# Kernel tuning notes

Hardware: AMD Instinct MI355X
Metric: run time of the kernel (lower is better)

The kernel has to match this reference:

```python
import jax, jax.numpy as jnp
import numpy as np

N = 50000   # total nodes in batched graph
E = 400000  # directed edges
G = 512     # number of graphs in batch
F = 128     # input node feature dim
K = 4       # attention heads
H = 64      # hidden feats per head (flatten width = K*H = 256)
EPS = 1e-5  # BatchNorm eps


def _edge_softmax(e, dst, n):
    # softmax of per-edge scores over incoming edges of each dst node; e: [E, K]
    m = jax.ops.segment_max(e, dst, num_segments=n)
    ee = jnp.exp(e - m[dst])
    s = jax.ops.segment_sum(ee, dst, num_segments=n)
    return ee / s[dst]


def _gat_layer(x, W, al, ar, b, resW, src, dst, agg):
    # dgl GATConv with residual=True, LeakyReLU(0.2), bias, ReLU activation
    n = x.shape[0]
    z = (x @ W).reshape(n, K, H)                      # [N, K, H]
    el = jnp.einsum('nkh,kh->nk', z, al)              # [N, K]
    er = jnp.einsum('nkh,kh->nk', z, ar)
    e = jax.nn.leaky_relu(el[src] + er[dst], negative_slope=0.2)  # [E, K]
    a = _edge_softmax(e, dst, n)                      # [E, K]
    rst = jax.ops.segment_sum(a[:, :, None] * z[src], dst, num_segments=n)  # [N, K, H]
    res = (x @ resW).reshape(n, K, H) if resW is not None else x.reshape(n, K, H)
    rst = jax.nn.relu(rst + res + b.reshape(1, K, H))
    return rst.reshape(n, K * H) if agg == 'flatten' else rst.mean(axis=1)


def setup_inputs() -> dict:
    key = jax.random.key(0)
    ks = jax.random.split(key, 16)
    f32 = jnp.float32

    def p(k, shape):
        return jax.random.normal(k, shape, f32) * 0.1

    h = jax.random.normal(ks[0], (N, F), f32)
    src = jax.random.randint(ks[1], (E,), 0, N)
    dst = jax.random.randint(ks[2], (E,), 0, N)
    graph_ids = (jnp.arange(N) * G) // N  # sorted node->graph assignment, all segments nonempty

    return dict(
        h=h, src=src, dst=dst, graph_ids=graph_ids,
        W0=p(ks[3], (F, K * H)), al0=p(ks[4], (K, H)), ar0=p(ks[5], (K, H)),
        b0=jnp.zeros((K * H,), f32), resW0=p(ks[6], (F, K * H)),
        W1=p(ks[7], (K * H, K * H)), al1=p(ks[8], (K, H)), ar1=p(ks[9], (K, H)),
        b1=jnp.zeros((K * H,), f32),
        W2=p(ks[10], (K * H, K * H)), al2=p(ks[11], (K, H)), ar2=p(ks[12], (K, H)),
        b2=jnp.zeros((K * H,), f32),
        Wg=p(ks[13], (H, 1)), bg=jnp.zeros((1,), f32),
        Wm1=p(ks[14], (2 * H, H)), bm1=jnp.zeros((H,), f32),
        bn_g=jnp.ones((H,), f32), bn_b=jnp.zeros((H,), f32),
        bn_m=jnp.zeros((H,), f32), bn_v=jnp.ones((H,), f32),
        Wm2=p(ks[15], (H, 1)), bm2=jnp.zeros((1,), f32),
    )


def reference(h, src, dst, graph_ids, W0, al0, ar0, b0, resW0, W1, al1, ar1, b1,
              W2, al2, ar2, b2, Wg, bg, Wm1, bm1, bn_g, bn_b, bn_m, bn_v, Wm2, bm2):
    # 3 GAT layers: flatten, flatten, mean (dgllife GATPredictor default agg modes)
    x = _gat_layer(h, W0, al0, ar0, b0, resW0, src, dst, 'flatten')   # [N, 256]
    x = _gat_layer(x, W1, al1, ar1, b1, None, src, dst, 'flatten')    # [N, 256] (identity residual)
    x = _gat_layer(x, W2, al2, ar2, b2, None, src, dst, 'mean')       # [N, 64]
    # WeightedSumAndMax readout
    w = jax.nn.sigmoid(x @ Wg + bg)                                   # [N, 1]
    gs = jax.ops.segment_sum(w * x, graph_ids, num_segments=G)        # [G, 64]
    gm = jax.ops.segment_max(x, graph_ids, num_segments=G)            # [G, 64]
    gf = jnp.concatenate([gs, gm], axis=1)                            # [G, 128]
    # MLPPredictor (eval mode: dropout off, BatchNorm uses running stats)
    y = jax.nn.relu(gf @ Wm1 + bm1)
    y = (y - bn_m) / jnp.sqrt(bn_v + EPS) * bn_g + bn_b
    out = jax.nn.sigmoid(y @ Wm2 + bm2)                               # [G, 1]
    return out
```

## Files before the change

kernel.cpp:

```cpp
#include <hip/hip_runtime.h>
#include <math.h>


typedef _Float16 f16;
typedef _Float16 f16x4 __attribute__((ext_vector_type(4)));
typedef _Float16 f16x8 __attribute__((ext_vector_type(8)));
typedef float f32x16 __attribute__((ext_vector_type(16)));

__device__ __forceinline__ double wred_sumd(double v) {
#pragma unroll
  for (int m = 32; m > 0; m >>= 1) v += __shfl_xor(v, m, 64);
  return v;
}

__global__ void k_hist(const int* __restrict__ dst, int* __restrict__ deg, int e) {
  int i = blockIdx.x * 256 + threadIdx.x;
  if (i < e) atomicAdd(&deg[dst[i]], 1);
}

__global__ void k_scan1(const int* __restrict__ deg, int* __restrict__ rowptr,
                        int* __restrict__ bsum, int n) {
  __shared__ int sh[256];
  int t = threadIdx.x;
  int base = blockIdx.x * 1024 + t * 4;
  int v0 = 0, v1 = 0, v2 = 0, v3 = 0;
  if (base + 0 < n) v0 = deg[base + 0];
  if (base + 1 < n) v1 = deg[base + 1];
  if (base + 2 < n) v2 = deg[base + 2];
  if (base + 3 < n) v3 = deg[base + 3];
  sh[t] = v0 + v1 + v2 + v3;
  __syncthreads();
  for (int off = 1; off < 256; off <<= 1) {
    int x = (t >= off) ? sh[t - off] : 0;
    __syncthreads();
    sh[t] += x;
    __syncthreads();
  }
  int excl = (t > 0) ? sh[t - 1] : 0;
  if (base + 0 < n) rowptr[base + 0] = excl;
  if (base + 1 < n) rowptr[base + 1] = excl + v0;
  if (base + 2 < n) rowptr[base + 2] = excl + v0 + v1;
  if (base + 3 < n) rowptr[base + 3] = excl + v0 + v1 + v2;
  if (t == 255) bsum[blockIdx.x] = sh[255];
}

__global__ void k_scan2(int* bsum, int nb) {
  if (threadIdx.x == 0 && blockIdx.x == 0) {
    int run = 0;
    for (int i = 0; i < nb; i++) { int v = bsum[i]; bsum[i] = run; run += v; }
  }
}

__global__ void k_scan3(int* __restrict__ rowptr, const int* __restrict__ bsum,
                        int n, int e) {
  int i = blockIdx.x * 256 + threadIdx.x;
  if (i < n) rowptr[i] += bsum[i >> 10];
  if (i == 0) rowptr[n] = e;
}

__global__ void k_scatter(const int* __restrict__ src, const int* __restrict__ dst,
                          const int* __restrict__ rowptr, int* __restrict__ cursor,
                          int* __restrict__ colsrc, int e) {
  int i = blockIdx.x * 256 + threadIdx.x;
  if (i < e) {
    int d = dst[i];
    int pos = rowptr[d] + atomicAdd(&cursor[d], 1);
    colsrc[pos] = src[i];
  }
}

__global__ __launch_bounds__(256) void k_split(const float* __restrict__ X,
                                               f16* __restrict__ X0,
                                               f16* __restrict__ X1, int n4) {
  int i = blockIdx.x * 256 + threadIdx.x;
  if (i >= n4) return;
  float4 v = *(const float4*)(X + (size_t)i * 4);
  f16x4 hi, lo;
  hi.x = (f16)v.x; lo.x = (f16)(v.x - (float)hi.x);
  hi.y = (f16)v.y; lo.y = (f16)(v.y - (float)hi.y);
  hi.z = (f16)v.z; lo.z = (f16)(v.z - (float)hi.z);
  hi.w = (f16)v.w; lo.w = (f16)(v.w - (float)hi.w);
  *(f16x4*)(X0 + (size_t)i * 4) = hi;
  *(f16x4*)(X1 + (size_t)i * 4) = lo;
}

__global__ void k_splitWT(const float* __restrict__ W, f16* __restrict__ P0,
                          f16* __restrict__ P1, int kin) {
  int c = blockIdx.x;
  for (int k = threadIdx.x; k < kin; k += blockDim.x) {
    float v = W[(size_t)k * 256 + c];
    f16 h0 = (f16)v;
    size_t off = ((size_t)(k >> 4) * 256 + c) * 16 + ((k >> 3) & 1) * 8 + (k & 7);
    P0[off] = h0;
    P1[off] = (f16)(v - (float)h0);
  }
}

template <int KIN, bool ELR>
__global__ __launch_bounds__(256) void k_gemm_mfma(
    const f16* __restrict__ X0, const f16* __restrict__ X1,
    const f16* __restrict__ WT0, const f16* __restrict__ WT1,
    float* __restrict__ C, const float* __restrict__ al,
    const float* __restrict__ ar, float* __restrict__ el,
    float* __restrict__ er, int M) {
  __shared__ f16 aLDS[2][2][64][8];
  const int t = threadIdx.x;
  const int w = t >> 6;
  const int lane = t & 63;
  const int lo = lane & 31, g = lane >> 5;
  const int row0 = blockIdx.x * 32;

  f32x16 acc0, acc1;
#pragma unroll
  for (int i = 0; i < 16; i++) { acc0[i] = 0.f; acc1[i] = 0.f; }

  const size_t fb0 = (size_t)(w * 64 + lo) * 16 + g * 8;
  const size_t fb1 = (size_t)(w * 64 + 32 + lo) * 16 + g * 8;

  for (int k0 = 0; k0 < KIN; k0 += 32) {
    if (k0) __syncthreads();
    {
      int s = t >> 7, r = (t >> 2) & 31, hh = t & 3;
      int kh = hh >> 1, gg = hh & 1;
      int gr = row0 + r;
      if (gr > M - 1) gr = M - 1;
      const f16* Xs = s ? X1 : X0;
      *(float4*)&aLDS[s][kh][(gg << 5) | r][0] =
          *(const float4*)&Xs[(size_t)gr * KIN + k0 + kh * 16 + gg * 8];
    }
    __syncthreads();
#pragma unroll
    for (int kh = 0; kh < 2; kh++) {
      const size_t bbase = (size_t)((k0 >> 4) + kh) * 4096;
      f16x8 a0 = *(const f16x8*)&aLDS[0][kh][lane][0];
      f16x8 a1 = *(const f16x8*)&aLDS[1][kh][lane][0];
      f16x8 b0c0 = *(const f16x8*)&WT0[bbase + fb0];
      f16x8 b0c1 = *(const f16x8*)&WT0[bbase + fb1];
      f16x8 b1c0 = *(const f16x8*)&WT1[bbase + fb0];
      f16x8 b1c1 = *(const f16x8*)&WT1[bbase + fb1];
      acc0 = __builtin_amdgcn_mfma_f32_32x32x16_f16(a0, b0c0, acc0, 0, 0, 0);
      acc1 = __builtin_amdgcn_mfma_f32_32x32x16_f16(a0, b0c1, acc1, 0, 0, 0);
      acc0 = __builtin_amdgcn_mfma_f32_32x32x16_f16(a0, b1c0, acc0, 0, 0, 0);
      acc1 = __builtin_amdgcn_mfma_f32_32x32x16_f16(a0, b1c1, acc1, 0, 0, 0);
      acc0 = __builtin_amdgcn_mfma_f32_32x32x16_f16(a1, b0c0, acc0, 0, 0, 0);
      acc1 = __builtin_amdgcn_mfma_f32_32x32x16_f16(a1, b0c1, acc1, 0, 0, 0);
    }
  }
  const int c0 = w * 64 + lo, c1 = w * 64 + 32 + lo;
#pragma unroll
  for (int reg = 0; reg < 16; reg++) {
    int rr = (reg & 3) + 8 * (reg >> 2) + 4 * g;
    int r0 = row0 + rr;
    if (r0 < M) {
      C[(size_t)r0 * 256 + c0] = acc0[reg];
      C[(size_t)r0 * 256 + c1] = acc1[reg];
    }
  }
  if (ELR) {
    __syncthreads();
    int r = t & 31, kk = (t >> 5) & 3, sel = t >> 7;
    int gr = row0 + r;
    if (gr < M) {
      const float* zr = C + (size_t)gr * 256 + kk * 64;
      const float* av = (sel ? ar : al) + kk * 64;
      float s = 0.f;
#pragma unroll
      for (int q = 0; q < 16; q++) {
        float4 zv = *(const float4*)(zr + q * 4);
        float4 a4 = *(const float4*)(av + q * 4);
        s += zv.x * a4.x + zv.y * a4.y + zv.z * a4.z + zv.w * a4.w;
      }
      (sel ? er : el)[gr * 4 + kk] = s;
    }
  }
}

template <int MEAN, int RESF16>
__global__ __launch_bounds__(256) void k_gather(
    const float* __restrict__ z, const float* __restrict__ el,
    const float* __restrict__ er, const float* __restrict__ resf,
    const f16* __restrict__ R0, const f16* __restrict__ R1,
    const float* __restrict__ bias, const int* __restrict__ rowptr,
    const int* __restrict__ colsrc, float* __restrict__ out,
    f16* __restrict__ O0, f16* __restrict__ O1, float* __restrict__ wn,
    const float* __restrict__ Wg, const float* __restrict__ bg, int n) {
  const int t = threadIdx.x;
  const int w = t >> 6, lane = t & 63;
  int node = blockIdx.x * 4 + w;
  if (node > n - 1) node = n - 1;
  const int base = rowptr[node];
  const int deg = rowptr[node + 1] - base;
  const int k = lane >> 4, j = lane & 15;
  const float ernk = er[node * 4 + k];

  float m = -INFINITY;
  for (int i0 = 0; i0 < deg; i0 += 16) {
    int i = i0 + j;
    if (i < deg) {
      int s = colsrc[base + i];
      float sc = el[s * 4 + k] + ernk;
      sc = (sc > 0.f) ? sc : 0.2f * sc;
      m = fmaxf(m, sc);
    }
  }
#pragma unroll
  for (int msk = 1; msk < 16; msk <<= 1) m = fmaxf(m, __shfl_xor(m, msk, 64));

  float ssum = 0.f;
  for (int i0 = 0; i0 < deg; i0 += 16) {
    int i = i0 + j;
    if (i < deg) {
      int s = colsrc[base + i];
      float sc = el[s * 4 + k] + ernk;
      sc = (sc > 0.f) ? sc : 0.2f * sc;
      ssum += expf(sc - m);
    }
  }
#pragma unroll
  for (int msk = 1; msk < 16; msk <<= 1) ssum += __shfl_xor(ssum, msk, 64);
  const float inv = 1.f / ssum;

  const char* zb = (const char*)z + lane * 16;
  float4 acc0 = {0, 0, 0, 0}, acc1 = {0, 0, 0, 0};
  float4 acc2 = {0, 0, 0, 0}, acc3 = {0, 0, 0, 0};
  int i = 0;
  for (; i + 4 <= deg; i += 4) {
    int s0 = colsrc[base + i + 0];
    int s1 = colsrc[base + i + 1];
    int s2 = colsrc[base + i + 2];
    int s3 = colsrc[base + i + 3];
    float4 z0 = *(const float4*)(zb + ((size_t)s0 << 10));
    float4 z1 = *(const float4*)(zb + ((size_t)s1 << 10));
    float4 z2 = *(const float4*)(zb + ((size_t)s2 << 10));
    float4 z3 = *(const float4*)(zb + ((size_t)s3 << 10));
    float c0 = el[s0 * 4 + k] + ernk; c0 = (c0 > 0.f) ? c0 : 0.2f * c0;
    float c1 = el[s1 * 4 + k] + ernk; c1 = (c1 > 0.f) ? c1 : 0.2f * c1;
    float c2 = el[s2 * 4 + k] + ernk; c2 = (c2 > 0.f) ? c2 : 0.2f * c2;
    float c3 = el[s3 * 4 + k] + ernk; c3 = (c3 > 0.f) ? c3 : 0.2f * c3;
    float a0 = expf(c0 - m) * inv;
    float a1 = expf(c1 - m) * inv;
    float a2 = expf(c2 - m) * inv;
    float a3 = expf(c3 - m) * inv;
    acc0.x = fmaf(a0, z0.x, acc0.x); acc0.y = fmaf(a0, z0.y, acc0.y);
    acc0.z = fmaf(a0, z0.z, acc0.z); acc0.w = fmaf(a0, z0.w, acc0.w);
    acc1.x = fmaf(a1, z1.x, acc1.x); acc1.y = fmaf(a1, z1.y, acc1.y);
    acc1.z = fmaf(a1, z1.z, acc1.z); acc1.w = fmaf(a1, z1.w, acc1.w);
    acc2.x = fmaf(a2, z2.x, acc2.x); acc2.y = fmaf(a2, z2.y, acc2.y);
    acc2.z = fmaf(a2, z2.z, acc2.z); acc2.w = fmaf(a2, z2.w, acc2.w);
    acc3.x = fmaf(a3, z3.x, acc3.x); acc3.y = fmaf(a3, z3.y, acc3.y);
    acc3.z = fmaf(a3, z3.z, acc3.z); acc3.w = fmaf(a3, z3.w, acc3.w);
  }
  for (; i < deg; i++) {
    int s = colsrc[base + i];
    float4 zv = *(const float4*)(zb + ((size_t)s << 10));
    float c = el[s * 4 + k] + ernk; c = (c > 0.f) ? c : 0.2f * c;
    float av = expf(c - m) * inv;
    acc0.x = fmaf(av, zv.x, acc0.x); acc0.y = fmaf(av, zv.y, acc0.y);
    acc0.z = fmaf(av, zv.z, acc0.z); acc0.w = fmaf(av, zv.w, acc0.w);
  }

  size_t o = (size_t)node * 256 + lane * 4;
  float4 rv;
  if (RESF16) {
    f16x4 rh = *(const f16x4*)(R0 + o);
    f16x4 rl = *(const f16x4*)(R1 + o);
    rv.x = (float)rh.x + (float)rl.x;
    rv.y = (float)rh.y + (float)rl.y;
    rv.z = (float)rh.z + (float)rl.z;
    rv.w = (float)rh.w + (float)rl.w;
  } else {
    rv = *(const float4*)(resf + o);
  }
  float4 bv = *(const float4*)(bias + lane * 4);
  float4 v;
  v.x = fmaxf(((acc0.x + acc1.x) + (acc2.x + acc3.x)) + rv.x + bv.x, 0.f);
  v.y = fmaxf(((acc0.y + acc1.y) + (acc2.y + acc3.y)) + rv.y + bv.y, 0.f);
  v.z = fmaxf(((acc0.z + acc1.z) + (acc2.z + acc3.z)) + rv.z + bv.z, 0.f);
  v.w = fmaxf(((acc0.w + acc1.w) + (acc2.w + acc3.w)) + rv.w + bv.w, 0.f);

  if (!MEAN) {
    f16x4 hi, lo;
    hi.x = (f16)v.x; lo.x = (f16)(v.x - (float)hi.x);
    hi.y = (f16)v.y; lo.y = (f16)(v.y - (float)hi.y);
    hi.z = (f16)v.z; lo.z = (f16)(v.z - (float)hi.z);
    hi.w = (f16)v.w; lo.w = (f16)(v.w - (float)hi.w);
    *(f16x4*)(O0 + o) = hi;
    *(f16x4*)(O1 + o) = lo;
  } else {
    __shared__ float tmp[4][256];
    *(float4*)&tmp[w][lane * 4] = v;
    __syncthreads();
    float xv = 0.25f * (tmp[w][lane] + tmp[w][lane + 64] + tmp[w][lane + 128] +
                        tmp[w][lane + 192]);
    out[(size_t)node * 64 + lane] = xv;
    double s = wred_sumd((double)xv * (double)Wg[lane]);
    if (lane == 0)
      wn[node] = (float)(1.0 / (1.0 + exp(-(s + (double)bg[0]))));
  }
}

__global__ __launch_bounds__(64) void k_readout(const float* __restrict__ x2,
                                                const float* __restrict__ wn,
                                                float* __restrict__ gf, int n,
                                                int g) {
  int gi = blockIdx.x;
  int lane = threadIdx.x;
  long long start = ((long long)gi * n + g - 1) / g;
  long long end = ((long long)(gi + 1) * n + g - 1) / g;
  double s = 0.0;
  float mx = -INFINITY;
  for (long long nd = start; nd < end; nd++) {
    float xv = x2[nd * 64 + lane];
    s += (double)wn[nd] * (double)xv;
    mx = fmaxf(mx, xv);
  }
  gf[gi * 128 + lane] = (float)s;
  gf[gi * 128 + 64 + lane] = mx;
}

__global__ __launch_bounds__(64) void k_mlp(const float* __restrict__ gf,
                                            const float* __restrict__ Wm1,
                                            const float* __restrict__ bm1,
                                            const float* __restrict__ bng,
                                            const float* __restrict__ bnb,
                                            const float* __restrict__ bnm,
                                            const float* __restrict__ bnv,
                                            const float* __restrict__ Wm2,
                                            const float* __restrict__ bm2,
                                            float* __restrict__ out) {
  int gi = blockIdx.x;
  int h = threadIdx.x;
  double y = (double)bm1[h];
  for (int i = 0; i < 128; i++)
    y += (double)gf[gi * 128 + i] * (double)Wm1[i * 64 + h];
  y = (y > 0.0) ? y : 0.0;
  y = (y - (double)bnm[h]) / sqrt((double)bnv[h] + 1e-5) * (double)bng[h] +
      (double)bnb[h];
  double v = wred_sumd(y * (double)Wm2[h]);
  if (h == 0) {
    double s = v + (double)bm2[0];
    out[gi] = (float)(1.0 / (1.0 + exp(-s)));
  }
}

extern "C" void kernel_launch(void* const* d_in, const int* in_sizes, int n_in,
                              void* d_out, int out_size, void* d_ws,
                              size_t ws_size, hipStream_t stream) {
  const float* h    = (const float*)d_in[0];
  const int*   src  = (const int*)d_in[1];
  const int*   dst  = (const int*)d_in[2];
  const float* W0    = (const float*)d_in[4];
  const float* al0   = (const float*)d_in[5];
  const float* ar0   = (const float*)d_in[6];
  const float* b0    = (const float*)d_in[7];
  const float* resW0 = (const float*)d_in[8];
  const float* W1    = (const float*)d_in[9];
  const float* al1   = (const float*)d_in[10];
  const float* ar1   = (const float*)d_in[11];
  const float* b1    = (const float*)d_in[12];
  const float* W2    = (const float*)d_in[13];
  const float* al2   = (const float*)d_in[14];
  const float* ar2   = (const float*)d_in[15];
  const float* b2    = (const float*)d_in[16];
  const float* Wg    = (const float*)d_in[17];
  const float* bg    = (const float*)d_in[18];
  const float* Wm1   = (const float*)d_in[19];
  const float* bm1   = (const float*)d_in[20];
  const float* bng   = (const float*)d_in[21];
  const float* bnb   = (const float*)d_in[22];
  const float* bnm   = (const float*)d_in[23];
  const float* bnv   = (const float*)d_in[24];
  const float* Wm2   = (const float*)d_in[25];
  const float* bm2   = (const float*)d_in[26];

  const int n = in_sizes[0] / 128;
  const int e = in_sizes[1];
  const int g = out_size;

  char* ws = (char*)d_ws;
  size_t off = 0;
  auto alloc = [&](size_t bytes) {
    void* p = ws + off;
    off += (bytes + 255) & ~(size_t)255;
    return p;
  };
  int*   deg    = (int*)alloc((size_t)n * 4);
  int*   cursor = (int*)alloc((size_t)n * 4);
  int*   rowptr = (int*)alloc((size_t)(n + 1) * 4);
  int*   bsum   = (int*)alloc(256 * 4);
  int*   colsrc = (int*)alloc((size_t)e * 4);
  float* el     = (float*)alloc((size_t)n * 4 * 4);
  float* er     = (float*)alloc((size_t)n * 4 * 4);
  float* bufA   = (float*)alloc((size_t)n * 256 * 4);
  float* bufB   = (float*)alloc((size_t)n * 256 * 4);
  float* x2     = (float*)alloc((size_t)n * 64 * 4);
  float* wn     = (float*)alloc((size_t)n * 4);
  float* gf     = (float*)alloc((size_t)g * 128 * 4);
  f16*   sA0    = (f16*)alloc((size_t)n * 256 * 2);
  f16*   sA1    = (f16*)alloc((size_t)n * 256 * 2);
  f16*   sB0    = (f16*)alloc((size_t)n * 256 * 2);
  f16*   sB1    = (f16*)alloc((size_t)n * 256 * 2);
  f16*   wtA0   = (f16*)alloc(65536 * 2);
  f16*   wtA1   = (f16*)alloc(65536 * 2);
  f16*   wtR0   = (f16*)alloc(65536 * 2);
  f16*   wtR1   = (f16*)alloc(65536 * 2);
  f16*   wtB0   = (f16*)alloc(65536 * 2);
  f16*   wtB1   = (f16*)alloc(65536 * 2);
  f16*   wtC0   = (f16*)alloc(65536 * 2);
  f16*   wtC1   = (f16*)alloc(65536 * 2);
  (void)ws_size;
  (void)n_in;

  hipMemsetAsync(deg, 0, (size_t)n * 4, stream);
  hipMemsetAsync(cursor, 0, (size_t)n * 4, stream);

  const int eb = (e + 255) / 256;
  const int nb = (n + 1023) / 1024;
  k_hist<<<eb, 256, 0, stream>>>(dst, deg, e);
  k_scan1<<<nb, 256, 0, stream>>>(deg, rowptr, bsum, n);
  k_scan2<<<1, 64, 0, stream>>>(bsum, nb);
  k_scan3<<<(n + 255) / 256, 256, 0, stream>>>(rowptr, bsum, n, e);
  k_scatter<<<eb, 256, 0, stream>>>(src, dst, rowptr, cursor, colsrc, e);

  k_splitWT<<<256, 256, 0, stream>>>(W0, wtA0, wtA1, 128);
  k_splitWT<<<256, 256, 0, stream>>>(resW0, wtR0, wtR1, 128);
  k_splitWT<<<256, 256, 0, stream>>>(W1, wtB0, wtB1, 256);
  k_splitWT<<<256, 256, 0, stream>>>(W2, wtC0, wtC1, 256);

  const int mb32 = (n + 31) / 32;
  const int n4 = (n + 3) / 4;
  const int sp128 = (n * 128 / 4 + 255) / 256;

  k_split<<<sp128, 256, 0, stream>>>(h, sA0, sA1, n * 128 / 4);
  k_gemm_mfma<128, true><<<mb32, 256, 0, stream>>>(sA0, sA1, wtA0, wtA1, bufA,
                                                   al0, ar0, el, er, n);
  k_gemm_mfma<128, false><<<mb32, 256, 0, stream>>>(
      sA0, sA1, wtR0, wtR1, bufB, nullptr, nullptr, nullptr, nullptr, n);
  k_gather<0, 0><<<n4, 256, 0, stream>>>(bufA, el, er, bufB, nullptr, nullptr,
                                         b0, rowptr, colsrc, nullptr, sB0, sB1,
                                         nullptr, nullptr, nullptr, n);

  k_gemm_mfma<256, true><<<mb32, 256, 0, stream>>>(sB0, sB1, wtB0, wtB1, bufA,
                                                   al1, ar1, el, er, n);
  k_gather<0, 1><<<n4, 256, 0, stream>>>(bufA, el, er, nullptr, sB0, sB1, b1,
                                         rowptr, colsrc, nullptr, sA0, sA1,
                                         nullptr, nullptr, nullptr, n);

  k_gemm_mfma<256, true><<<mb32, 256, 0, stream>>>(sA0, sA1, wtC0, wtC1, bufA,
                                                   al2, ar2, el, er, n);
  k_gather<1, 1><<<n4, 256, 0, stream>>>(bufA, el, er, nullptr, sA0, sA1, b2,
                                         rowptr, colsrc, x2, nullptr, nullptr,
                                         wn, Wg, bg, n);

  k_readout<<<g, 64, 0, stream>>>(x2, wn, gf, n, g);
  k_mlp<<<g, 64, 0, stream>>>(gf, Wm1, bm1, bng, bnb, bnm, bnv, Wm2, bm2,
                              (float*)d_out);
}
```

Measured before the change: 488.0 us.

## Fuse layer-0 projection and residual GEMMs, widen K-step, use online softmax

Merges the layer-0 feature projection and residual projection into one kernel, so the split-fp16 input tile is loaded once and feeds both weight sets. The GEMM K-step grows from 32 to 64, halving the number of barrier-separated iterations at the cost of a larger LDS tile. The gather kernel replaces its two passes over the edge scores (max, then sum of exponentials) with one online-softmax pass, removing a second read of colsrc and el but adding an extra exp per edge. The fused kernel carries four accumulator sets, which raises register pressure.

```diff
diff --git a/kernel.cpp b/kernel.cpp
--- a/kernel.cpp
+++ b/kernel.cpp
@@ -103,7 +103,7 @@
     float* __restrict__ C, const float* __restrict__ al,
     const float* __restrict__ ar, float* __restrict__ el,
     float* __restrict__ er, int M) {
-  __shared__ f16 aLDS[2][2][64][8];
+  __shared__ f16 aLDS[2][4][64][8];
   const int t = threadIdx.x;
   const int w = t >> 6;
   const int lane = t & 63;
@@ -117,11 +117,14 @@
   const size_t fb0 = (size_t)(w * 64 + lo) * 16 + g * 8;
   const size_t fb1 = (size_t)(w * 64 + 32 + lo) * 16 + g * 8;
 
-  for (int k0 = 0; k0 < KIN; k0 += 32) {
+  for (int k0 = 0; k0 < KIN; k0 += 64) {
     if (k0) __syncthreads();
-    {
-      int s = t >> 7, r = (t >> 2) & 31, hh = t & 3;
-      int kh = hh >> 1, gg = hh & 1;
+#pragma unroll
+    for (int ii = 0; ii < 2; ii++) {
+      int c = t + ii * 256;
+      int s = c >> 8, cc = c & 255;
+      int r = cc >> 3, hc = cc & 7;
+      int kh = hc >> 1, gg = hc & 1;
       int gr = row0 + r;
       if (gr > M - 1) gr = M - 1;
       const f16* Xs = s ? X1 : X0;
@@ -130,7 +133,7 @@
     }
     __syncthreads();
 #pragma unroll
-    for (int kh = 0; kh < 2; kh++) {
+    for (int kh = 0; kh < 4; kh++) {
       const size_t bbase = (size_t)((k0 >> 4) + kh) * 4096;
       f16x8 a0 = *(const f16x8*)&aLDS[0][kh][lane][0];
       f16x8 a1 = *(const f16x8*)&aLDS[1][kh][lane][0];
@@ -172,6 +175,101 @@
       }
       (sel ? er : el)[gr * 4 + kk] = s;
     }
+  }
+}
+
+__global__ __launch_bounds__(256) void k_gemm_mfma2(
+    const f16* __restrict__ X0, const f16* __restrict__ X1,
+    const f16* __restrict__ Wa0, const f16* __restrict__ Wa1,
+    const f16* __restrict__ Wb0, const f16* __restrict__ Wb1,
+    float* __restrict__ Ca, float* __restrict__ Cb,
+    const float* __restrict__ al, const float* __restrict__ ar,
+    float* __restrict__ el, float* __restrict__ er, int M) {
+  const int KIN = 128;
+  __shared__ f16 aLDS[2][4][64][8];
+  const int t = threadIdx.x;
+  const int w = t >> 6;
+  const int lane = t & 63;
+  const int lo = lane & 31, g = lane >> 5;
+  const int row0 = blockIdx.x * 32;
+
+  f32x16 accA0, accA1, accB0, accB1;
+#pragma unroll
+  for (int i = 0; i < 16; i++) {
+    accA0[i] = 0.f; accA1[i] = 0.f; accB0[i] = 0.f; accB1[i] = 0.f;
+  }
+
+  const size_t fb0 = (size_t)(w * 64 + lo) * 16 + g * 8;
+  const size_t fb1 = (size_t)(w * 64 + 32 + lo) * 16 + g * 8;
+
+  for (int k0 = 0; k0 < KIN; k0 += 64) {
+    if (k0) __syncthreads();
+#pragma unroll
+    for (int ii = 0; ii < 2; ii++) {
+      int c = t + ii * 256;
+      int s = c >> 8, cc = c & 255;
+      int r = cc >> 3, hc = cc & 7;
+      int kh = hc >> 1, gg = hc & 1;
+      int gr = row0 + r;
+      if (gr > M - 1) gr = M - 1;
+      const f16* Xs = s ? X1 : X0;
+      *(float4*)&aLDS[s][kh][(gg << 5) | r][0] =
+          *(const float4*)&Xs[(size_t)gr * KIN + k0 + kh * 16 + gg * 8];
+    }
+    __syncthreads();
+#pragma unroll
+    for (int kh = 0; kh < 4; kh++) {
+      const size_t bbase = (size_t)((k0 >> 4) + kh) * 4096;
+      f16x8 a0 = *(const f16x8*)&aLDS[0][kh][lane][0];
+      f16x8 a1 = *(const f16x8*)&aLDS[1][kh][lane][0];
+      f16x8 pa0 = *(const f16x8*)&Wa0[bbase + fb0];
+      f16x8 pa1 = *(const f16x8*)&Wa0[bbase + fb1];
+      f16x8 qa0 = *(const f16x8*)&Wa1[bbase + fb0];
+      f16x8 qa1 = *(const f16x8*)&Wa1[bbase + fb1];
+      accA0 = __builtin_amdgcn_mfma_f32_32x32x16_f16(a0, pa0, accA0, 0, 0, 0);
+      accA1 = __builtin_amdgcn_mfma_f32_32x32x16_f16(a0, pa1, accA1, 0, 0, 0);
+      accA0 = __builtin_amdgcn_mfma_f32_32x32x16_f16(a0, qa0, accA0, 0, 0, 0);
+      accA1 = __builtin_amdgcn_mfma_f32_32x32x16_f16(a0, qa1, accA1, 0, 0, 0);
+      accA0 = __builtin_amdgcn_mfma_f32_32x32x16_f16(a1, pa0, accA0, 0, 0, 0);
+      accA1 = __builtin_amdgcn_mfma_f32_32x32x16_f16(a1, pa1, accA1, 0, 0, 0);
+      f16x8 pb0 = *(const f16x8*)&Wb0[bbase + fb0];
+      f16x8 pb1 = *(const f16x8*)&Wb0[bbase + fb1];
+      f16x8 qb0 = *(const f16x8*)&Wb1[bbase + fb0];
+      f16x8 qb1 = *(const f16x8*)&Wb1[bbase + fb1];
+      accB0 = __builtin_amdgcn_mfma_f32_32x32x16_f16(a0, pb0, accB0, 0, 0, 0);
+      accB1 = __builtin_amdgcn_mfma_f32_32x32x16_f16(a0, pb1, accB1, 0, 0, 0);
+      accB0 = __builtin_amdgcn_mfma_f32_32x32x16_f16(a0, qb0, accB0, 0, 0, 0);
+      accB1 = __builtin_amdgcn_mfma_f32_32x32x16_f16(a0, qb1, accB1, 0, 0, 0);
+      accB0 = __builtin_amdgcn_mfma_f32_32x32x16_f16(a1, pb0, accB0, 0, 0, 0);
+      accB1 = __builtin_amdgcn_mfma_f32_32x32x16_f16(a1, pb1, accB1, 0, 0, 0);
+    }
+  }
+  const int c0 = w * 64 + lo, c1 = w * 64 + 32 + lo;
+#pragma unroll
+  for (int reg = 0; reg < 16; reg++) {
+    int rr = (reg & 3) + 8 * (reg >> 2) + 4 * g;
+    int r0 = row0 + rr;
+    if (r0 < M) {
+      Ca[(size_t)r0 * 256 + c0] = accA0[reg];
+      Ca[(size_t)r0 * 256 + c1] = accA1[reg];
+      Cb[(size_t)r0 * 256 + c0] = accB0[reg];
+      Cb[(size_t)r0 * 256 + c1] = accB1[reg];
+    }
+  }
+  __syncthreads();
+  int r = t & 31, kk = (t >> 5) & 3, sel = t >> 7;
+  int gr = row0 + r;
+  if (gr < M) {
+    const float* zr = Ca + (size_t)gr * 256 + kk * 64;
+    const float* av = (sel ? ar : al) + kk * 64;
+    float s = 0.f;
+#pragma unroll
+    for (int q = 0; q < 16; q++) {
+      float4 zv = *(const float4*)(zr + q * 4);
+      float4 a4 = *(const float4*)(av + q * 4);
+      s += zv.x * a4.x + zv.y * a4.y + zv.z * a4.z + zv.w * a4.w;
+    }
+    (sel ? er : el)[gr * 4 + kk] = s;
   }
 }
 
@@ -193,29 +291,22 @@
   const int k = lane >> 4, j = lane & 15;
   const float ernk = er[node * 4 + k];
 
-  float m = -INFINITY;
+  float mj = -INFINITY, sj = 0.f;
   for (int i0 = 0; i0 < deg; i0 += 16) {
     int i = i0 + j;
     if (i < deg) {
       int s = colsrc[base + i];
       float sc = el[s * 4 + k] + ernk;
       sc = (sc > 0.f) ? sc : 0.2f * sc;
-      m = fmaxf(m, sc);
-    }
-  }
+      float mn = fmaxf(mj, sc);
+      sj = sj * expf(mj - mn) + expf(sc - mn);
+      mj = mn;
+    }
+  }
+  float m = mj;
 #pragma unroll
   for (int msk = 1; msk < 16; msk <<= 1) m = fmaxf(m, __shfl_xor(m, msk, 64));
-
-  float ssum = 0.f;
-  for (int i0 = 0; i0 < deg; i0 += 16) {
-    int i = i0 + j;
-    if (i < deg) {
-      int s = colsrc[base + i];
-      float sc = el[s * 4 + k] + ernk;
-      sc = (sc > 0.f) ? sc : 0.2f * sc;
-      ssum += expf(sc - m);
-    }
-  }
+  float ssum = sj * expf(mj - m);
 #pragma unroll
   for (int msk = 1; msk < 16; msk <<= 1) ssum += __shfl_xor(ssum, msk, 64);
   const float inv = 1.f / ssum;
@@ -432,10 +523,8 @@
   const int sp128 = (n * 128 / 4 + 255) / 256;
 
   k_split<<<sp128, 256, 0, stream>>>(h, sA0, sA1, n * 128 / 4);
-  k_gemm_mfma<128, true><<<mb32, 256, 0, stream>>>(sA0, sA1, wtA0, wtA1, bufA,
-                                                   al0, ar0, el, er, n);
-  k_gemm_mfma<128, false><<<mb32, 256, 0, stream>>>(
-      sA0, sA1, wtR0, wtR1, bufB, nullptr, nullptr, nullptr, nullptr, n);
+  k_gemm_mfma2<<<mb32, 256, 0, stream>>>(sA0, sA1, wtA0, wtA1, wtR0, wtR1,
+                                         bufA, bufB, al0, ar0, el, er, n);
   k_gather<0, 0><<<n4, 256, 0, stream>>>(bufA, el, er, bufB, nullptr, nullptr,
                                          b0, rowptr, colsrc, nullptr, sB0, sB1,
                                          nullptr, nullptr, nullptr, n);
```

Result: slower. 506.9 us (+3.9%).
